# Kernel tuning notes

Measured on AMD Instinct MI355X. Metric: run time of the kernel, lower is better.

The kernel has to match this reference:

```python
import jax, jax.numpy as jnp
import numpy as np

B, NX, NY, T = 8, 512, 512, 2_000_000


def setup_inputs() -> dict:
    key = jax.random.key(0)
    k1, k2, k3 = jax.random.split(key, 3)
    # regular source grid (flattened row-major: flat = j*NX + i, x varies fastest)
    xs = jnp.linspace(0.0, 1.0, NX, dtype=jnp.float32)
    ys = jnp.linspace(0.0, 1.0, NY, dtype=jnp.float32)
    SX, SY = jnp.meshgrid(xs, ys)  # (NY, NX)
    src_x = SX.reshape(1, -1)
    src_y = SY.reshape(1, -1)
    # target points strictly inside the convex hull (no NaN extrapolation)
    eps = 1e-3
    tgt_x = jax.random.uniform(k1, (1, T), jnp.float32, eps, 1.0 - eps)
    tgt_y = jax.random.uniform(k2, (1, T), jnp.float32, eps, 1.0 - eps)
    x = jax.random.normal(k3, (B, NX * NY, 1), jnp.float32)
    return {"x": x, "src_x": src_x, "src_y": src_y,
            "tgt_x": tgt_x, "tgt_y": tgt_y, "nx": NX, "ny": NY}


def reference(x, src_x, src_y, tgt_x, tgt_y, nx, ny):
    # Linear ND (triangulated) interpolation of x from a regular source grid
    # onto scattered target points. Each grid cell is split along the
    # (i,j)-(i+1,j+1) diagonal; barycentric weights inside each triangle.
    sx = src_x.reshape(-1)
    sy = src_y.reshape(-1)
    tx = tgt_x.reshape(-1)
    ty = tgt_y.reshape(-1)
    x0, x1 = sx.min(), sx.max()
    y0, y1 = sy.min(), sy.max()
    dx = (x1 - x0) / (nx - 1)
    dy = (y1 - y0) / (ny - 1)
    fx = (tx - x0) / dx
    fy = (ty - y0) / dy
    ix = jnp.clip(jnp.floor(fx), 0, nx - 2)
    iy = jnp.clip(jnp.floor(fy), 0, ny - 2)
    u = fx - ix  # local cell coords in [0,1]
    v = fy - iy
    ii = jax.lax.stop_gradient(ix).astype(jnp.int32)
    jj = jax.lax.stop_gradient(iy).astype(jnp.int32)
    base = jj * nx + ii
    i00, i10, i01, i11 = base, base + 1, base + nx, base + nx + 1
    lower = (u + v) <= 1.0  # which triangle of the cell
    idx = jnp.where(lower[:, None],
                    jnp.stack([i00, i10, i01], axis=-1),
                    jnp.stack([i11, i10, i01], axis=-1))  # [t,3]
    w = jnp.where(lower[:, None],
                  jnp.stack([1.0 - u - v, u, v], axis=-1),
                  jnp.stack([u + v - 1.0, 1.0 - v, 1.0 - u], axis=-1))  # [t,3]
    vals = x[:, idx, 0]                      # [b,t,3] gather of triangle vertices
    out = jnp.einsum('btk,tk->bt', vals, w)  # barycentric combination
    return out[..., None]                    # [b,t,1]
```

## Files before the change

kernel.cpp:

```cpp
#include <hip/hip_runtime.h>
#include <hip/hip_fp16.h>


typedef float  f32x4 __attribute__((ext_vector_type(4)));
typedef unsigned int u32x4 __attribute__((ext_vector_type(4)));

union HalfPack8 { __half h[8]; u32x4 u; };

__global__ __launch_bounds__(256) void build_records_kernel(
    const float* __restrict__ x,
    u32x4* __restrict__ rec,
    const int* __restrict__ nx_p,
    int N)
{
    const int nx = *nx_p;
    const int ny = N / nx;
    const int ncx = nx - 1;
    const int ncells = ncx * (ny - 1);
    int c = blockIdx.x * blockDim.x + threadIdx.x;
    if (c >= ncells) return;
    int i = c % ncx;
    int j = c / ncx;
    long base = (long)j * nx + i;

    HalfPack8 p00, p10, p01, p11;
    #pragma unroll
    for (int b = 0; b < 8; ++b) {
        const float* xb = x + (long)b * N;
        p00.h[b] = __float2half(xb[base]);
        p10.h[b] = __float2half(xb[base + 1]);
        p01.h[b] = __float2half(xb[base + nx]);
        p11.h[b] = __float2half(xb[base + nx + 1]);
    }
    u32x4* dst = rec + (long)c * 4;
    dst[0] = p00.u;
    dst[1] = p10.u;
    dst[2] = p01.u;
    dst[3] = p11.u;
}

__device__ __forceinline__ void half8_to_float8(u32x4 u, float* f) {
    union { u32x4 v; __half2 h2[4]; } cv;
    cv.v = u;
    float2 a = __half22float2(cv.h2[0]); f[0] = a.x; f[1] = a.y;
    float2 b = __half22float2(cv.h2[1]); f[2] = b.x; f[3] = b.y;
    float2 c = __half22float2(cv.h2[2]); f[4] = c.x; f[5] = c.y;
    float2 d = __half22float2(cv.h2[3]); f[6] = d.x; f[7] = d.y;
}

__global__ __launch_bounds__(256, 2) void interp_rec_kernel(
    const u32x4* __restrict__ rec,
    const float* __restrict__ src_x,
    const float* __restrict__ src_y,
    const float* __restrict__ tgt_x,
    const float* __restrict__ tgt_y,
    const int* __restrict__ nx_p,
    float* __restrict__ out,
    int T, int N)
{
    const int nx = *nx_p;
    const int ny = N / nx;
    const int ncx = nx - 1;
    const float x0 = src_x[0];
    const float x1 = src_x[nx - 1];
    const float y0 = src_y[0];
    const float y1 = src_y[N - 1];
    const float dx = (x1 - x0) / (float)(nx - 1);
    const float dy = (y1 - y0) / (float)(ny - 1);

    const int t0 = (blockIdx.x * blockDim.x + threadIdx.x) * 4;
    if (t0 >= T) return;

    if (t0 + 4 <= T) {
        f32x4 tx4 = __builtin_nontemporal_load(
            reinterpret_cast<const f32x4*>(tgt_x + t0));
        f32x4 ty4 = __builtin_nontemporal_load(
            reinterpret_cast<const f32x4*>(tgt_y + t0));

        const u32x4* p0[4];
        const u32x4* p1[4];
        const u32x4* p2[4];
        float w0a[4], w1a[4], w2a[4];
        #pragma unroll
        for (int k = 0; k < 4; ++k) {
            float fx = (tx4[k] - x0) / dx;
            float fy = (ty4[k] - y0) / dy;
            float ix = fminf(fmaxf(floorf(fx), 0.0f), (float)(nx - 2));
            float iy = fminf(fmaxf(floorf(fy), 0.0f), (float)(ny - 2));
            float u = fx - ix;
            float v = fy - iy;
            bool lower = (u + v) <= 1.0f;
            int c = (int)iy * ncx + (int)ix;
            const u32x4* r = rec + (long)c * 4;
            p0[k] = r + (lower ? 0 : 3);
            p1[k] = r + 1;
            p2[k] = r + 2;
            w0a[k] = lower ? (1.0f - u - v) : (u + v - 1.0f);
            w1a[k] = lower ? u : (1.0f - v);
            w2a[k] = lower ? v : (1.0f - u);
        }

        u32x4 r0[4], r1[4], r2[4];
        #pragma unroll
        for (int k = 0; k < 4; ++k) { r0[k] = *p0[k]; }
        #pragma unroll
        for (int k = 0; k < 4; ++k) { r1[k] = *p1[k]; }
        #pragma unroll
        for (int k = 0; k < 4; ++k) { r2[k] = *p2[k]; }

        float res[4][8];
        #pragma unroll
        for (int k = 0; k < 4; ++k) {
            float f0[8], f1[8], f2[8];
            half8_to_float8(r0[k], f0);
            half8_to_float8(r1[k], f1);
            half8_to_float8(r2[k], f2);
            #pragma unroll
            for (int b = 0; b < 8; ++b)
                res[k][b] = f0[b] * w0a[k] + f1[b] * w1a[k] + f2[b] * w2a[k];
        }

        #pragma unroll
        for (int b = 0; b < 8; ++b) {
            f32x4 r4 = { res[0][b], res[1][b], res[2][b], res[3][b] };
            __builtin_nontemporal_store(
                r4, reinterpret_cast<f32x4*>(out + (long)b * T + t0));
        }
    } else {
        for (int t = t0; t < T; ++t) {
            float fx = (tgt_x[t] - x0) / dx;
            float fy = (tgt_y[t] - y0) / dy;
            float ix = fminf(fmaxf(floorf(fx), 0.0f), (float)(nx - 2));
            float iy = fminf(fmaxf(floorf(fy), 0.0f), (float)(ny - 2));
            float u = fx - ix;
            float v = fy - iy;
            bool lower = (u + v) <= 1.0f;
            int c = (int)iy * ncx + (int)ix;
            const u32x4* r = rec + (long)c * 4;
            u32x4 q0 = r[lower ? 0 : 3], q1 = r[1], q2 = r[2];
            float w0 = lower ? (1.0f - u - v) : (u + v - 1.0f);
            float w1 = lower ? u : (1.0f - v);
            float w2 = lower ? v : (1.0f - u);
            float f0[8], f1[8], f2[8];
            half8_to_float8(q0, f0);
            half8_to_float8(q1, f1);
            half8_to_float8(q2, f2);
            for (int b = 0; b < 8; ++b)
                out[(long)b * T + t] = f0[b] * w0 + f1[b] * w1 + f2[b] * w2;
        }
    }
}

__global__ __launch_bounds__(256) void interp_fallback_kernel(
    const float* __restrict__ x,
    const float* __restrict__ src_x,
    const float* __restrict__ src_y,
    const float* __restrict__ tgt_x,
    const float* __restrict__ tgt_y,
    const int* __restrict__ nx_p,
    float* __restrict__ out,
    int T, int N, int B)
{
    const int nx = *nx_p;
    const int ny = N / nx;
    const float x0 = src_x[0];
    const float x1 = src_x[nx - 1];
    const float y0 = src_y[0];
    const float y1 = src_y[N - 1];
    const float dx = (x1 - x0) / (float)(nx - 1);
    const float dy = (y1 - y0) / (float)(ny - 1);

    const int t = blockIdx.x * blockDim.x + threadIdx.x;
    if (t >= T) return;
    float fx = (tgt_x[t] - x0) / dx;
    float fy = (tgt_y[t] - y0) / dy;
    float ix = fminf(fmaxf(floorf(fx), 0.0f), (float)(nx - 2));
    float iy = fminf(fmaxf(floorf(fy), 0.0f), (float)(ny - 2));
    float u = fx - ix;
    float v = fy - iy;
    int base = (int)iy * nx + (int)ix;
    bool lower = (u + v) <= 1.0f;
    int   i0 = lower ? base : (base + nx + 1);
    int   i1 = base + 1;
    int   i2 = base + nx;
    float w0 = lower ? (1.0f - u - v) : (u + v - 1.0f);
    float w1 = lower ? u : (1.0f - v);
    float w2 = lower ? v : (1.0f - u);
    for (int b = 0; b < B; ++b) {
        const float* xb = x + (long)b * N;
        out[(long)b * T + t] = xb[i0] * w0 + xb[i1] * w1 + xb[i2] * w2;
    }
}

extern "C" void kernel_launch(void* const* d_in, const int* in_sizes, int n_in,
                              void* d_out, int out_size, void* d_ws, size_t ws_size,
                              hipStream_t stream) {
    const float* x     = (const float*)d_in[0];
    const float* src_x = (const float*)d_in[1];
    const float* src_y = (const float*)d_in[2];
    const float* tgt_x = (const float*)d_in[3];
    const float* tgt_y = (const float*)d_in[4];
    const int*   nx_p  = (const int*)d_in[5];
    float* out = (float*)d_out;

    const int N = in_sizes[1];
    const int T = in_sizes[3];
    const int B = in_sizes[0] / N;

    const size_t rec_bytes = (size_t)N * 64;

    if (B == 8 && ws_size >= rec_bytes) {
        u32x4* rec = (u32x4*)d_ws;
        {
            const int block = 256;
            const int grid = (N + block - 1) / block;
            build_records_kernel<<<grid, block, 0, stream>>>(x, rec, nx_p, N);
        }
        {
            const int threads_needed = (T + 3) / 4;
            const int block = 256;
            const int grid = (threads_needed + block - 1) / block;
            interp_rec_kernel<<<grid, block, 0, stream>>>(
                rec, src_x, src_y, tgt_x, tgt_y, nx_p, out, T, N);
        }
    } else {
        const int block = 256;
        const int grid = (T + block - 1) / block;
        interp_fallback_kernel<<<grid, block, 0, stream>>>(
            x, src_x, src_y, tgt_x, tgt_y, nx_p, out, T, N, B);
    }
}
```

Measured before the change: 136.7 us.

## Replace per-cell 4-corner records with per-gridpoint half8 records

The preprocessing now packs each grid point's 8 batch values into one 16-byte fp16 record, instead of duplicating all four corners per cell into 64-byte records. The build kernel reads x with vectorized loads and writes a quarter as much data. The interpolation kernel indexes the point grid directly for its three triangle vertices. This cuts build-kernel write traffic and workspace footprint, and the smaller table should cache better, at the cost of gathers being spread over two rows instead of one contiguous record.

After: 129.4 us. -5.4%, faster.

```diff
diff --git a/kernel.cpp b/kernel.cpp
--- a/kernel.cpp
+++ b/kernel.cpp
@@ -5,38 +5,42 @@
 typedef float  f32x4 __attribute__((ext_vector_type(4)));
 typedef unsigned int u32x4 __attribute__((ext_vector_type(4)));
 
-union HalfPack8 { __half h[8]; u32x4 u; };
-
-__global__ __launch_bounds__(256) void build_records_kernel(
+__device__ __forceinline__ unsigned pack_h2(float lo, float hi) {
+    union { __half2 h2; unsigned u; } cv;
+    cv.h2 = __float22half2_rn(make_float2(lo, hi));
+    return cv.u;
+}
+
+__global__ __launch_bounds__(256) void build_grid16(
     const float* __restrict__ x,
     u32x4* __restrict__ rec,
-    const int* __restrict__ nx_p,
     int N)
 {
-    const int nx = *nx_p;
-    const int ny = N / nx;
-    const int ncx = nx - 1;
-    const int ncells = ncx * (ny - 1);
-    int c = blockIdx.x * blockDim.x + threadIdx.x;
-    if (c >= ncells) return;
-    int i = c % ncx;
-    int j = c / ncx;
-    long base = (long)j * nx + i;
-
-    HalfPack8 p00, p10, p01, p11;
-    #pragma unroll
-    for (int b = 0; b < 8; ++b) {
-        const float* xb = x + (long)b * N;
-        p00.h[b] = __float2half(xb[base]);
-        p10.h[b] = __float2half(xb[base + 1]);
-        p01.h[b] = __float2half(xb[base + nx]);
-        p11.h[b] = __float2half(xb[base + nx + 1]);
-    }
-    u32x4* dst = rec + (long)c * 4;
-    dst[0] = p00.u;
-    dst[1] = p10.u;
-    dst[2] = p01.u;
-    dst[3] = p11.u;
+    const int p0 = (blockIdx.x * blockDim.x + threadIdx.x) * 4;
+    if (p0 + 4 <= N) {
+        f32x4 v[8];
+        #pragma unroll
+        for (int b = 0; b < 8; ++b)
+            v[b] = *reinterpret_cast<const f32x4*>(x + (long)b * N + p0);
+        #pragma unroll
+        for (int k = 0; k < 4; ++k) {
+            u32x4 r;
+            r[0] = pack_h2(v[0][k], v[1][k]);
+            r[1] = pack_h2(v[2][k], v[3][k]);
+            r[2] = pack_h2(v[4][k], v[5][k]);
+            r[3] = pack_h2(v[6][k], v[7][k]);
+            rec[p0 + k] = r;
+        }
+    } else {
+        for (int p = p0; p < N; ++p) {
+            u32x4 r;
+            r[0] = pack_h2(x[p], x[(long)N + p]);
+            r[1] = pack_h2(x[2L * N + p], x[3L * N + p]);
+            r[2] = pack_h2(x[4L * N + p], x[5L * N + p]);
+            r[3] = pack_h2(x[6L * N + p], x[7L * N + p]);
+            rec[p] = r;
+        }
+    }
 }
 
 __device__ __forceinline__ void half8_to_float8(u32x4 u, float* f) {
@@ -60,7 +64,6 @@
 {
     const int nx = *nx_p;
     const int ny = N / nx;
-    const int ncx = nx - 1;
     const float x0 = src_x[0];
     const float x1 = src_x[nx - 1];
     const float y0 = src_y[0];
@@ -90,11 +93,10 @@
             float u = fx - ix;
             float v = fy - iy;
             bool lower = (u + v) <= 1.0f;
-            int c = (int)iy * ncx + (int)ix;
-            const u32x4* r = rec + (long)c * 4;
-            p0[k] = r + (lower ? 0 : 3);
-            p1[k] = r + 1;
-            p2[k] = r + 2;
+            int g = (int)iy * nx + (int)ix;
+            p0[k] = rec + g + (lower ? 0 : (nx + 1));
+            p1[k] = rec + g + 1;
+            p2[k] = rec + g + nx;
             w0a[k] = lower ? (1.0f - u - v) : (u + v - 1.0f);
             w1a[k] = lower ? u : (1.0f - v);
             w2a[k] = lower ? v : (1.0f - u);
@@ -135,9 +137,10 @@
             float u = fx - ix;
             float v = fy - iy;
             bool lower = (u + v) <= 1.0f;
-            int c = (int)iy * ncx + (int)ix;
-            const u32x4* r = rec + (long)c * 4;
-            u32x4 q0 = r[lower ? 0 : 3], q1 = r[1], q2 = r[2];
+            int g = (int)iy * nx + (int)ix;
+            u32x4 q0 = rec[g + (lower ? 0 : (nx + 1))];
+            u32x4 q1 = rec[g + 1];
+            u32x4 q2 = rec[g + nx];
             float w0 = lower ? (1.0f - u - v) : (u + v - 1.0f);
             float w1 = lower ? u : (1.0f - v);
             float w2 = lower ? v : (1.0f - u);
@@ -207,14 +210,14 @@
     const int T = in_sizes[3];
     const int B = in_sizes[0] / N;
 
-    const size_t rec_bytes = (size_t)N * 64;
+    const size_t rec_bytes = (size_t)N * 16;
 
     if (B == 8 && ws_size >= rec_bytes) {
         u32x4* rec = (u32x4*)d_ws;
         {
             const int block = 256;
-            const int grid = (N + block - 1) / block;
-            build_records_kernel<<<grid, block, 0, stream>>>(x, rec, nx_p, N);
+            const int grid = ((N + 3) / 4 + block - 1) / block;
+            build_grid16<<<grid, block, 0, stream>>>(x, rec, N);
         }
         {
             const int threads_needed = (T + 3) / 4;
```
